# Performance work log

Hardware: AMD Instinct MI355X
Metric: run time of the kernel (lower is better)

The kernel has to match this reference:

```python
import jax, jax.numpy as jnp
import numpy as np

NUM_HEADS = 12
SEQ_H = 32
SEQ_W = 32
D_HALF = 32
ROPE_BASE = 10000.0
LN_EPS = 1e-5


def build_rope_cache(seq_len, head_dim, base=ROPE_BASE):
    inv_freq = 1.0 / base ** (jnp.arange(0, head_dim, 2, dtype=jnp.float32) / head_dim)
    t = jnp.arange(seq_len, dtype=jnp.float32)
    freqs = jnp.outer(t, inv_freq)  # [seq_len, head_dim//2]
    cos = jnp.repeat(jnp.cos(freqs), 2, axis=-1)  # [seq_len, head_dim]
    sin = jnp.repeat(jnp.sin(freqs), 2, axis=-1)
    return cos, sin


def apply_rope(x, cos, sin):
    # x: [B,H,N,d_sub], cos/sin: [N,d_sub]
    x_even, x_odd = x[..., ::2], x[..., 1::2]
    x_rot = jnp.stack([-x_odd, x_even], axis=-1).reshape(x.shape)
    return x * cos[None, None] + x_rot * sin[None, None]


def setup_inputs() -> dict:
    key = jax.random.key(0)
    ks = jax.random.split(key, 3)
    B, N, D = 8, 1025, 768
    return {
        "x": jax.random.normal(ks[0], (B, N, D), dtype=jnp.float32),
        "ln_g": jnp.ones((D,), dtype=jnp.float32),
        "ln_b": jnp.zeros((D,), dtype=jnp.float32),
        "w_qkv": jax.random.normal(ks[1], (3 * D, D), dtype=jnp.float32) * 0.02,
        "w_proj": jax.random.normal(ks[2], (D, D), dtype=jnp.float32) * 0.02,
        "b_proj": jnp.zeros((D,), dtype=jnp.float32),
    }


def reference(x, ln_g, ln_b, w_qkv, w_proj, b_proj):
    B, N, D = x.shape
    H = NUM_HEADS
    hd = D // H
    d2 = D_HALF
    scale = hd ** -0.5

    # LayerNorm
    mu = jnp.mean(x, axis=-1, keepdims=True)
    var = jnp.mean(jnp.square(x - mu), axis=-1, keepdims=True)
    xn = (x - mu) * jax.lax.rsqrt(var + LN_EPS) * ln_g + ln_b

    # QKV projection (no bias)
    qkv = jnp.einsum("bnd,ed->bne", xn, w_qkv).reshape(B, N, 3, H, hd)
    qkv = jnp.transpose(qkv, (2, 0, 3, 1, 4))  # [3,B,H,N,hd]
    q, k, v = qkv[0], qkv[1], qkv[2]

    # 2D position ids (CLS token -> row 0, col 0)
    patch_lin = jnp.arange(N - 1)
    rows = patch_lin // SEQ_W
    cols = patch_lin % SEQ_W
    zero = jnp.zeros((1,), dtype=patch_lin.dtype)
    row_ids = jnp.concatenate([zero, rows])
    col_ids = jnp.concatenate([zero, cols])

    cos_row, sin_row = build_rope_cache(SEQ_H, d2)
    cos_col, sin_col = build_rope_cache(SEQ_W, d2)
    cos_r, sin_r = cos_row[row_ids], sin_row[row_ids]  # [N,d2]
    cos_c, sin_c = cos_col[col_ids], sin_col[col_ids]

    q = jnp.concatenate(
        [apply_rope(q[..., :d2], cos_r, sin_r), apply_rope(q[..., d2:], cos_c, sin_c)], axis=-1)
    k = jnp.concatenate(
        [apply_rope(k[..., :d2], cos_r, sin_r), apply_rope(k[..., d2:], cos_c, sin_c)], axis=-1)

    attn = jnp.einsum("bhqd,bhkd->bhqk", q, k) * scale
    attn = jax.nn.softmax(attn, axis=-1)
    out = jnp.einsum("bhqk,bhkd->bhqd", attn, v)  # [B,H,N,hd]
    out = jnp.transpose(out, (0, 2, 1, 3)).reshape(B, N, D)
    return jnp.einsum("bnd,ed->bne", out, w_proj) + b_proj
```

## Files before the change

kernel.cpp:

```cpp
#include <hip/hip_runtime.h>
#include <hip/hip_bf16.h>

typedef unsigned short u16;

#define B_      8
#define N_      1025
#define D_      768
#define H_      12
#define HD_     64
#define M_REAL  (B_ * N_)
#define M_PAD   8320
#define QKVC    (3 * D_)

typedef __attribute__((ext_vector_type(8))) short bf16x8;
typedef __attribute__((ext_vector_type(4))) float f32x4;

static __device__ __forceinline__ float bf2f(u16 u) {
    union { unsigned int i; float f; } v; v.i = ((unsigned int)u) << 16; return v.f;
}
static __device__ __forceinline__ u16 f2bf(float f) {
    union { float f; unsigned int i; } v; v.f = f;
    unsigned int x = v.i;
    return (u16)((x + 0x7fffu + ((x >> 16) & 1u)) >> 16);
}
static __device__ __forceinline__ unsigned int cvtpk(float a, float b) {
    unsigned int r;
    asm volatile("v_cvt_pk_bf16_f32 %0, %1, %2" : "=v"(r) : "v"(a), "v"(b));
    return r;
}

static __device__ __forceinline__ void g2l16(const u16* g, u16* l) {
    __builtin_amdgcn_global_load_lds(
        (const __attribute__((address_space(1))) unsigned int*)g,
        (__attribute__((address_space(3))) unsigned int*)l, 16, 0, 0);
}

__global__ __launch_bounds__(256)
void ln_f2b_kernel(const float* __restrict__ x, const float* __restrict__ g,
                   const float* __restrict__ bvec, u16* __restrict__ xn,
                   const float* __restrict__ wq, u16* __restrict__ wqb,
                   const float* __restrict__ wp, u16* __restrict__ wpb)
{
    const int tid = threadIdx.x;
    if (blockIdx.x >= M_REAL) {
        int i = (blockIdx.x - M_REAL) * 1024 + tid * 4;
        const float* src; u16* dst;
        if (i < QKVC * D_) { src = wq + i; dst = wqb + i; }
        else { src = wp + (i - QKVC * D_); dst = wpb + (i - QKVC * D_); }
        float4 v = *(const float4*)src;
        dst[0] = f2bf(v.x); dst[1] = f2bf(v.y);
        dst[2] = f2bf(v.z); dst[3] = f2bf(v.w);
        return;
    }
    const int row = blockIdx.x;
    const float* xr = x + (size_t)row * D_;
    float v[3];
    float s = 0.f, ss = 0.f;
#pragma unroll
    for (int j = 0; j < 3; j++) {
        float val = xr[tid + j * 256];
        v[j] = val; s += val; ss += val * val;
    }
    __shared__ float r1[256], r2[256];
    r1[tid] = s; r2[tid] = ss; __syncthreads();
    for (int off = 128; off > 0; off >>= 1) {
        if (tid < off) { r1[tid] += r1[tid + off]; r2[tid] += r2[tid + off]; }
        __syncthreads();
    }
    const float mean = r1[0] * (1.0f / D_);
    const float var  = r2[0] * (1.0f / D_) - mean * mean;
    const float rs   = rsqrtf(var + 1e-5f);
    u16* outr = xn + (size_t)row * D_;
#pragma unroll
    for (int j = 0; j < 3; j++) {
        int c = tid + j * 256;
        outr[c] = f2bf((v[j] - mean) * rs * g[c] + bvec[c]);
    }
}

template <typename OutT, bool ROPE>
__global__ __launch_bounds__(256)
void gemm_bt(const u16* __restrict__ A, const u16* __restrict__ B,
             OutT* __restrict__ C, const float* __restrict__ bias,
             int M_real, int Ncols, int K,
             int BM, int BN, int gh, int gw, int PC)
{
    const int l   = blockIdx.x;
    const int xcd = l & 7;
    const int i0  = l >> 3;
    const int pr  = xcd / PC, pc = xcd % PC;
    const int bm  = pr * gh + (i0 % gh);
    const int bn  = pc * gw + (i0 / gh);
    if (bm >= BM || bn >= BN) return;

    __shared__ __align__(16) unsigned char smem[34816];
    u16* As0 = (u16*)smem;
    u16* Bs0 = (u16*)(smem + 8192);
    u16*   ep16 = (u16*)smem;
    float* ep32 = (float*)smem;

    const int tid  = threadIdx.x;
    const int wave = tid >> 6, lane = tid & 63;
    const int wm   = (wave >> 1) * 64, wn = (wave & 1) * 64;
    const int lrow = lane & 15, lq = lane >> 4;
    const int lrow4 = lane >> 2, lchunk = lane & 3;

    int ar0 = bm * 128 + wave * 16 + lrow4;       if (ar0 >= M_real) ar0 = M_real - 1;
    int ar1 = bm * 128 + (wave + 4) * 16 + lrow4; if (ar1 >= M_real) ar1 = M_real - 1;
    const u16* apg0 = A + (size_t)ar0 * K + lchunk * 8;
    const u16* apg1 = A + (size_t)ar1 * K + lchunk * 8;
    const u16* bpg0 = B + (size_t)(bn * 128 + wave * 16 + lrow4) * K + lchunk * 8;
    const u16* bpg1 = B + (size_t)(bn * 128 + (wave + 4) * 16 + lrow4) * K + lchunk * 8;
    u16* asl0 = As0 + wave * 512;       u16* asl1 = As0 + (wave + 4) * 512;
    u16* bsl0 = Bs0 + wave * 512;       u16* bsl1 = Bs0 + (wave + 4) * 512;
    const int bufoff = 8192;

    f32x4 acc[4][4];
#pragma unroll
    for (int i = 0; i < 4; i++)
#pragma unroll
        for (int j = 0; j < 4; j++)
            acc[i][j] = (f32x4){0.f, 0.f, 0.f, 0.f};

    g2l16(apg0, asl0); g2l16(apg1, asl1);
    g2l16(bpg0, bsl0); g2l16(bpg1, bsl1);

    const int kTiles = K / 32;
    for (int kt = 0; kt < kTiles; kt++) {
        const int cur = kt & 1;
        __syncthreads();
        if (kt + 1 < kTiles) {
            const int k1 = (kt + 1) * 32;
            const int no = (cur ^ 1) * bufoff;
            g2l16(apg0 + k1, asl0 + no); g2l16(apg1 + k1, asl1 + no);
            g2l16(bpg0 + k1, bsl0 + no); g2l16(bpg1 + k1, bsl1 + no);
        }
        const u16* Asr = As0 + cur * bufoff;
        const u16* Bsr = Bs0 + cur * bufoff;
        bf16x8 af[4], bfr[4];
#pragma unroll
        for (int i = 0; i < 4; i++) {
            af[i]  = *(const bf16x8*)&Asr[(wm + i * 16 + lrow) * 32 + lq * 8];
            bfr[i] = *(const bf16x8*)&Bsr[(wn + i * 16 + lrow) * 32 + lq * 8];
        }
#pragma unroll
        for (int i = 0; i < 4; i++)
#pragma unroll
            for (int j = 0; j < 4; j++)
                acc[i][j] = __builtin_amdgcn_mfma_f32_16x16x32_bf16(af[i], bfr[j], acc[i][j], 0, 0, 0);
    }
    __syncthreads();

    if constexpr (sizeof(OutT) == 2) {
#pragma unroll
        for (int j = 0; j < 4; j++) {
            int gcol = bn * 128 + wn + j * 16 + lrow;
            float bv = bias ? bias[gcol] : 0.f;
            int qk = gcol / D_;
            int dh = gcol & 63;
            int half = dh >> 5, ii = (dh & 31) >> 1;
            float sgn = (dh & 1) ? 1.f : -1.f;
            float invf = exp2f(-(float)ii * 0.8304820237218406f);
#pragma unroll
            for (int i = 0; i < 4; i++)
#pragma unroll
                for (int r = 0; r < 4; r++) {
                    int grow = bm * 128 + wm + i * 16 + lq * 4 + r;
                    float val = acc[i][j][r] + bv;
                    if constexpr (ROPE) {
                        if (qk < 2) {
                            float partner = __shfl_xor(val, 1);
                            int n = grow % N_;
                            int pl = n - 1;
                            int pos = (n == 0) ? 0 : (half ? (pl & 31) : (pl >> 5));
                            float ang = (float)pos * invf;
                            val = val * __cosf(ang) + sgn * partner * __sinf(ang);
                            if (qk == 0) val *= 0.125f;
                        }
                    }
                    ep16[(wm + i * 16 + lq * 4 + r) * 136 + wn + j * 16 + lrow] = f2bf(val);
                }
        }
        __syncthreads();
#pragma unroll
        for (int c = 0; c < 8; c++) {
            int idx = tid + c * 256;
            int row = idx >> 4, l16 = idx & 15;
            int grow = bm * 128 + row;
            if (grow < M_real)
                *(uint4*)((u16*)C + (size_t)grow * Ncols + bn * 128 + l16 * 8) =
                    *(const uint4*)&ep16[row * 136 + l16 * 8];
        }
    } else {
#pragma unroll
        for (int s = 0; s < 2; s++) {
            if (s) __syncthreads();
            if (wm == s * 64) {
#pragma unroll
                for (int j = 0; j < 4; j++) {
                    int gcol = bn * 128 + wn + j * 16 + lrow;
                    float bv = bias ? bias[gcol] : 0.f;
#pragma unroll
                    for (int i = 0; i < 4; i++)
#pragma unroll
                        for (int r = 0; r < 4; r++)
                            ep32[(i * 16 + lq * 4 + r) * 132 + wn + j * 16 + lrow] =
                                acc[i][j][r] + bv;
                }
            }
            __syncthreads();
#pragma unroll
            for (int c = 0; c < 8; c++) {
                int idx = tid + c * 256;
                int row = idx >> 5, l32 = idx & 31;
                int grow = bm * 128 + s * 64 + row;
                if (grow < M_real)
                    *(uint4*)((float*)C + (size_t)grow * Ncols + bn * 128 + l32 * 4) =
                        *(const uint4*)&ep32[row * 132 + l32 * 4];
            }
        }
    }
}

__global__ __launch_bounds__(256)
void attn_mfma(const u16* __restrict__ qkv, u16* __restrict__ out)
{
    __shared__ __align__(16) u16 Kt[2][64][72];
    __shared__ __align__(16) u16 Vt[2][64][72];
    __shared__ float Lw[4][32];

    const int l   = blockIdx.x;
    const int xcd = l & 7;
    const int j0  = l >> 3;
    const int bh  = xcd * 12 + j0 / 9;
    const int b  = bh / H_, h = bh % H_;
    const int q0 = (j0 % 9) * 128;
    const int tid  = threadIdx.x;
    const int wave = tid >> 6, lane = tid & 63;
    const int lm = lane & 15, lq = lane >> 4;
    const int qw = q0 + wave * 32;

    const int vcol = (lane & 35) | ((lane & 12) << 1) | ((lane & 16) >> 2);

    bf16x8 qf[2][2];
#pragma unroll
    for (int sq = 0; sq < 2; sq++) {
        int qrow = qw + sq * 16 + lm; if (qrow > N_ - 1) qrow = N_ - 1;
        const u16* qptr = qkv + (size_t)(b * N_ + qrow) * QKVC + h * HD_;
        qf[sq][0] = *(const bf16x8*)(qptr + lq * 8);
        qf[sq][1] = *(const bf16x8*)(qptr + 32 + lq * 8);
    }

    float l_r[2] = {0.f, 0.f};
    f32x4 o_acc[2][4];
#pragma unroll
    for (int sq = 0; sq < 2; sq++)
#pragma unroll
        for (int t = 0; t < 4; t++)
            o_acc[sq][t] = (f32x4){0.f, 0.f, 0.f, 0.f};

    bf16x8 kreg[2], vreg[2];
    {
        int krow = lane; if (krow > N_ - 1) krow = N_ - 1;
        const u16* kvp = qkv + (size_t)(b * N_ + krow) * QKVC + h * HD_;
#pragma unroll
        for (int p = 0; p < 2; p++) {
            int dg = wave + p * 4;
            kreg[p] = *(const bf16x8*)(kvp + D_ + dg * 8);
            vreg[p] = *(const bf16x8*)(kvp + 2 * D_ + dg * 8);
        }
    }

    const int kTiles = (N_ + 63) / 64;
    for (int kt = 0; kt < kTiles; kt++) {
        const int kbase = kt * 64;
        const int buf = kt & 1;

#pragma unroll
        for (int pp = 0; pp < 2; pp++) {
            int dg = wave + pp * 4;
            *(bf16x8*)&Kt[buf][lane][dg * 8] = kreg[pp];
#pragma unroll
            for (int j = 0; j < 8; j++)
                Vt[buf][dg * 8 + j][vcol] = (u16)vreg[pp][j];
        }

        if (kt + 1 < kTiles) {
            int krow = kbase + 64 + lane; if (krow > N_ - 1) krow = N_ - 1;
            const u16* kvp = qkv + (size_t)(b * N_ + krow) * QKVC + h * HD_;
#pragma unroll
            for (int pp = 0; pp < 2; pp++) {
                int dg = wave + pp * 4;
                kreg[pp] = *(const bf16x8*)(kvp + D_ + dg * 8);
                vreg[pp] = *(const bf16x8*)(kvp + 2 * D_ + dg * 8);
            }
        }

        asm volatile("s_waitcnt lgkmcnt(0)" ::: "memory");
        __builtin_amdgcn_s_barrier();

        f32x4 sc[2][4];
        __builtin_amdgcn_s_setprio(1);
#pragma unroll
        for (int st = 0; st < 4; st++) {
            bf16x8 kf0 = *(const bf16x8*)&Kt[buf][st * 16 + lm][lq * 8];
            bf16x8 kf1 = *(const bf16x8*)&Kt[buf][st * 16 + lm][32 + lq * 8];
#pragma unroll
            for (int sq = 0; sq < 2; sq++) {
                f32x4 s4 = (f32x4){0.f, 0.f, 0.f, 0.f};
                s4 = __builtin_amdgcn_mfma_f32_16x16x32_bf16(kf0, qf[sq][0], s4, 0, 0, 0);
                s4 = __builtin_amdgcn_mfma_f32_16x16x32_bf16(kf1, qf[sq][1], s4, 0, 0, 0);
                sc[sq][st] = s4;
            }
        }
        __builtin_amdgcn_s_setprio(0);

        const bool lastT = (kt == kTiles - 1);
        bf16x8 pa[2][2];
#pragma unroll
        for (int sq = 0; sq < 2; sq++) {
            union { bf16x8 v; unsigned int u[4]; } pk0, pk1;
#pragma unroll
            for (int st = 0; st < 4; st++) {
                float p0 = __expf(sc[sq][st][0]);
                float p1 = __expf(sc[sq][st][1]);
                float p2 = __expf(sc[sq][st][2]);
                float p3 = __expf(sc[sq][st][3]);
                if (lastT) {
                    const int keyb = kbase + st * 16 + lq * 4;
                    if (keyb + 0 >= N_) p0 = 0.f;
                    if (keyb + 1 >= N_) p1 = 0.f;
                    if (keyb + 2 >= N_) p2 = 0.f;
                    if (keyb + 3 >= N_) p3 = 0.f;
                }
                l_r[sq] += (p0 + p1) + (p2 + p3);
                unsigned int lo = cvtpk(p0, p1);
                unsigned int hi = cvtpk(p2, p3);
                if      (st == 0) { pk0.u[0] = lo; pk0.u[1] = hi; }
                else if (st == 1) { pk0.u[2] = lo; pk0.u[3] = hi; }
                else if (st == 2) { pk1.u[0] = lo; pk1.u[1] = hi; }
                else              { pk1.u[2] = lo; pk1.u[3] = hi; }
            }
            pa[sq][0] = pk0.v; pa[sq][1] = pk1.v;
        }

        __builtin_amdgcn_s_setprio(1);
#pragma unroll
        for (int nt = 0; nt < 4; nt++) {
            bf16x8 vb0 = *(const bf16x8*)&Vt[buf][nt * 16 + lm][lq * 8];
            bf16x8 vb1 = *(const bf16x8*)&Vt[buf][nt * 16 + lm][32 + lq * 8];
#pragma unroll
            for (int sq = 0; sq < 2; sq++) {
                o_acc[sq][nt] = __builtin_amdgcn_mfma_f32_16x16x32_bf16(pa[sq][0], vb0, o_acc[sq][nt], 0, 0, 0);
                o_acc[sq][nt] = __builtin_amdgcn_mfma_f32_16x16x32_bf16(pa[sq][1], vb1, o_acc[sq][nt], 0, 0, 0);
            }
        }
        __builtin_amdgcn_s_setprio(0);
    }

#pragma unroll
    for (int sq = 0; sq < 2; sq++) {
        float l2 = l_r[sq];
        l2 += __shfl_xor(l2, 16);
        l2 += __shfl_xor(l2, 32);
        if (lq == 0) Lw[wave][sq * 16 + lm] = l2;
    }
    asm volatile("s_waitcnt lgkmcnt(0)" ::: "memory");

#pragma unroll
    for (int sq = 0; sq < 2; sq++)
#pragma unroll
        for (int r = 0; r < 4; r++) {
            int q = qw + sq * 16 + lq * 4 + r;
            if (q < N_) {
                float inv = 1.0f / Lw[wave][sq * 16 + lq * 4 + r];
                u16* orow = out + (size_t)(b * N_ + q) * D_ + h * HD_ + lm;
#pragma unroll
                for (int nt = 0; nt < 4; nt++)
                    orow[nt * 16] = f2bf(o_acc[sq][nt][r] * inv);
            }
        }
}

extern "C" void kernel_launch(void* const* d_in, const int* in_sizes, int n_in,
                              void* d_out, int out_size, void* d_ws, size_t ws_size,
                              hipStream_t stream)
{
    const float* x      = (const float*)d_in[0];
    const float* ln_g   = (const float*)d_in[1];
    const float* ln_b   = (const float*)d_in[2];
    const float* w_qkv  = (const float*)d_in[3];
    const float* w_proj = (const float*)d_in[4];
    const float* b_proj = (const float*)d_in[5];

    u16* wqkv_b  = (u16*)d_ws;
    u16* wproj_b = wqkv_b + (size_t)QKVC * D_;
    u16* xn      = wproj_b + (size_t)D_ * D_;
    u16* qkv     = xn + (size_t)M_PAD * D_;
    u16* attno   = xn;

    ln_f2b_kernel<<<M_REAL + (QKVC * D_ + D_ * D_) / 1024, 256, 0, stream>>>(
        x, ln_g, ln_b, xn, w_qkv, wqkv_b, w_proj, wproj_b);

    gemm_bt<u16, true><<<1224, 256, 0, stream>>>(
        xn, wqkv_b, qkv, nullptr, M_REAL, QKVC, D_,
        65, 18, 17, 9, 2);

    attn_mfma<<<864, 256, 0, stream>>>(qkv, attno);

    gemm_bt<float, false><<<432, 256, 0, stream>>>(
        attno, wproj_b, (float*)d_out, b_proj, M_REAL, D_, D_,
        65, 6, 9, 6, 1);
}
```

Measured before the change: 214.7 us.

## Use wave-per-row LayerNorm and explicit vmcnt barriers in GEMM loop

LayerNorm now assigns one row per wavefront, using vectorized float4 loads and stores and an xor-shuffle reduction in place of the shared-memory tree with many __syncthreads. The GEMM k-loop replaces __syncthreads with explicit s_waitcnt vmcnt plus s_barrier, so the prefetch for the next tile can stay in flight while the current tile is consumed. It also raises wave priority around the MFMA block. The change adds a second barrier per iteration and depends on the vmcnt counts being correct.

```diff
diff --git a/kernel.cpp b/kernel.cpp
--- a/kernel.cpp
+++ b/kernel.cpp
@@ -11,6 +11,7 @@
 #define M_REAL  (B_ * N_)
 #define M_PAD   8320
 #define QKVC    (3 * D_)
+#define LN_BLK  (M_REAL / 4)
 
 typedef __attribute__((ext_vector_type(8))) short bf16x8;
 typedef __attribute__((ext_vector_type(4))) float f32x4;
@@ -42,8 +43,8 @@
                    const float* __restrict__ wp, u16* __restrict__ wpb)
 {
     const int tid = threadIdx.x;
-    if (blockIdx.x >= M_REAL) {
-        int i = (blockIdx.x - M_REAL) * 1024 + tid * 4;
+    if (blockIdx.x >= LN_BLK) {
+        int i = (blockIdx.x - LN_BLK) * 1024 + tid * 4;
         const float* src; u16* dst;
         if (i < QKVC * D_) { src = wq + i; dst = wqb + i; }
         else { src = wp + (i - QKVC * D_); dst = wpb + (i - QKVC * D_); }
@@ -52,29 +53,38 @@
         dst[2] = f2bf(v.z); dst[3] = f2bf(v.w);
         return;
     }
-    const int row = blockIdx.x;
+    const int wave = tid >> 6, lane = tid & 63;
+    const int row  = blockIdx.x * 4 + wave;
     const float* xr = x + (size_t)row * D_;
-    float v[3];
+    float4 v[3];
     float s = 0.f, ss = 0.f;
 #pragma unroll
     for (int j = 0; j < 3; j++) {
-        float val = xr[tid + j * 256];
-        v[j] = val; s += val; ss += val * val;
-    }
-    __shared__ float r1[256], r2[256];
-    r1[tid] = s; r2[tid] = ss; __syncthreads();
-    for (int off = 128; off > 0; off >>= 1) {
-        if (tid < off) { r1[tid] += r1[tid + off]; r2[tid] += r2[tid + off]; }
-        __syncthreads();
-    }
-    const float mean = r1[0] * (1.0f / D_);
-    const float var  = r2[0] * (1.0f / D_) - mean * mean;
+        float4 t = *(const float4*)&xr[j * 256 + lane * 4];
+        v[j] = t;
+        s  += (t.x + t.y) + (t.z + t.w);
+        ss += (t.x * t.x + t.y * t.y) + (t.z * t.z + t.w * t.w);
+    }
+#pragma unroll
+    for (int off = 1; off < 64; off <<= 1) {
+        s  += __shfl_xor(s,  off);
+        ss += __shfl_xor(ss, off);
+    }
+    const float mean = s * (1.0f / D_);
+    const float var  = ss * (1.0f / D_) - mean * mean;
     const float rs   = rsqrtf(var + 1e-5f);
     u16* outr = xn + (size_t)row * D_;
 #pragma unroll
     for (int j = 0; j < 3; j++) {
-        int c = tid + j * 256;
-        outr[c] = f2bf((v[j] - mean) * rs * g[c] + bvec[c]);
+        int c = j * 256 + lane * 4;
+        float4 g4 = *(const float4*)&g[c];
+        float4 b4 = *(const float4*)&bvec[c];
+        u16 o[4];
+        o[0] = f2bf((v[j].x - mean) * rs * g4.x + b4.x);
+        o[1] = f2bf((v[j].y - mean) * rs * g4.y + b4.y);
+        o[2] = f2bf((v[j].z - mean) * rs * g4.z + b4.z);
+        o[3] = f2bf((v[j].w - mean) * rs * g4.w + b4.w);
+        *(uint2*)&outr[c] = *(const uint2*)o;
     }
 }
 
@@ -128,13 +138,17 @@
     const int kTiles = K / 32;
     for (int kt = 0; kt < kTiles; kt++) {
         const int cur = kt & 1;
-        __syncthreads();
         if (kt + 1 < kTiles) {
             const int k1 = (kt + 1) * 32;
             const int no = (cur ^ 1) * bufoff;
             g2l16(apg0 + k1, asl0 + no); g2l16(apg1 + k1, asl1 + no);
             g2l16(bpg0 + k1, bsl0 + no); g2l16(bpg1 + k1, bsl1 + no);
-        }
+            asm volatile("s_waitcnt vmcnt(4)" ::: "memory");
+        } else {
+            asm volatile("s_waitcnt vmcnt(0)" ::: "memory");
+        }
+        __builtin_amdgcn_s_barrier();
+
         const u16* Asr = As0 + cur * bufoff;
         const u16* Bsr = Bs0 + cur * bufoff;
         bf16x8 af[4], bfr[4];
@@ -143,11 +157,14 @@
             af[i]  = *(const bf16x8*)&Asr[(wm + i * 16 + lrow) * 32 + lq * 8];
             bfr[i] = *(const bf16x8*)&Bsr[(wn + i * 16 + lrow) * 32 + lq * 8];
         }
+        __builtin_amdgcn_s_setprio(1);
 #pragma unroll
         for (int i = 0; i < 4; i++)
 #pragma unroll
             for (int j = 0; j < 4; j++)
                 acc[i][j] = __builtin_amdgcn_mfma_f32_16x16x32_bf16(af[i], bfr[j], acc[i][j], 0, 0, 0);
+        __builtin_amdgcn_s_setprio(0);
+        __builtin_amdgcn_s_barrier();
     }
     __syncthreads();
 
@@ -399,7 +416,7 @@
     u16* qkv     = xn + (size_t)M_PAD * D_;
     u16* attno   = xn;
 
-    ln_f2b_kernel<<<M_REAL + (QKVC * D_ + D_ * D_) / 1024, 256, 0, stream>>>(
+    ln_f2b_kernel<<<LN_BLK + (QKVC * D_ + D_ * D_) / 1024, 256, 0, stream>>>(
         x, ln_g, ln_b, xn, w_qkv, wqkv_b, w_proj, wproj_b);
 
     gemm_bt<u16, true><<<1224, 256, 0, stream>>>(
```

New measurement: 211.8 us. No clear change (-1.3%).
